# Optimization experiments

Measured on AMD Instinct MI355X. Metric: run time of the kernel, lower is better.

## Reference

```python
import jax, jax.numpy as jnp
import numpy as np

B, E, H, T, O = 128, 512, 1024, 256, 512  # H = 2*E per module


def _uniform(key, shape, k):
    return jax.random.uniform(key, shape, jnp.float32, -k, k)


def setup_inputs() -> dict:
    key = jax.random.key(0)
    ks = jax.random.split(key, 8)
    k_lstm = 1.0 / np.sqrt(H)
    k_fc = 1.0 / np.sqrt(H)
    return {
        "x": jax.random.normal(ks[0], (B, E), jnp.float32),
        "W_ih": _uniform(ks[1], (4 * H, E), k_lstm),   # torch weight_ih_l0, gate order i,f,g,o
        "W_hh": _uniform(ks[2], (4 * H, H), k_lstm),   # torch weight_hh_l0
        "b_ih": _uniform(ks[3], (4 * H,), k_lstm),
        "b_hh": _uniform(ks[4], (4 * H,), k_lstm),
        "fc_w": _uniform(ks[5], (O, H), k_fc),
        "fc_b": _uniform(ks[6], (O,), k_fc),
        "sequence_length": T,
    }


def _lstm_const_input(x, W_ih, W_hh, b_ih, b_hh, T):
    """Single-layer LSTM over `x` repeated T times. Input projection is
    constant across steps, so precompute it once (the headroom insight)."""
    Bb = x.shape[0]
    Hh = W_hh.shape[1]
    z = x @ W_ih.T + (b_ih + b_hh)  # [B, 4H], same every step

    def step(carry, _):
        h, c = carry
        gates = z + h @ W_hh.T                      # [B, 4H]
        i, f, g, o = jnp.split(gates, 4, axis=-1)   # torch gate order i,f,g,o
        i = jax.nn.sigmoid(i)
        f = jax.nn.sigmoid(f)
        g = jnp.tanh(g)
        o = jax.nn.sigmoid(o)
        c = f * c + i * g
        h = o * jnp.tanh(c)
        return (h, c), h

    h0 = jnp.zeros((Bb, Hh), x.dtype)
    (hT, cT), hs = jax.lax.scan(step, (h0, h0), None, length=T)
    return hs, hT  # hs: [T, B, H]


def reference(x, W_ih, W_hh, b_ih, b_hh, fc_w, fc_b, sequence_length):
    hs, hT = _lstm_const_input(x, W_ih, W_hh, b_ih, b_hh, sequence_length)
    seq = jnp.transpose(hs, (1, 0, 2))              # [B, T, H]
    out_sequence = seq @ fc_w.T + fc_b              # [B, T, O]
    # torch: h has shape [num_layers=1, B, H]; h[:, -1, :] picks last batch elem -> [1, H]
    next_state = hT[-1][None, :]
    return out_sequence, next_state
```

## Files before the change

### kernel.cpp

```cpp
#include <hip/hip_runtime.h>
#include <cstdint>
#include <cstddef>

#define BB 128
#define EE 512
#define HH 1024
#define G4 4096
#define OO 512
#define NBLKP 128
#define NTHR 512
#define RED36 36
#define SMEM_BYTES (131072 + BB * RED36 * 4)
#define SPIN_LIMIT (1u << 16)
#define FLAGSTRIDE 16

typedef float f32x4 __attribute__((ext_vector_type(4)));
typedef short s16x8 __attribute__((ext_vector_type(8)));
typedef __bf16 b16x8 __attribute__((ext_vector_type(8)));

template <typename V>
__device__ __forceinline__ auto mfma_try(V a, V b, f32x4 c, int)
    -> decltype(__builtin_amdgcn_mfma_f32_16x16x32_bf16(a, b, c, 0, 0, 0)) {
  return __builtin_amdgcn_mfma_f32_16x16x32_bf16(a, b, c, 0, 0, 0);
}
template <typename V>
__device__ __forceinline__ f32x4 mfma_try(V a, V b, f32x4 c, long) {
  b16x8 ab = __builtin_bit_cast(b16x8, a);
  b16x8 bb = __builtin_bit_cast(b16x8, b);
  return __builtin_amdgcn_mfma_f32_16x16x32_bf16(ab, bb, c, 0, 0, 0);
}
__device__ __forceinline__ f32x4 mfma_bf16(s16x8 a, s16x8 b, f32x4 c) {
  return mfma_try(a, b, c, 0);
}

__device__ __forceinline__ float bf2f(ushort s) {
  unsigned int u = ((unsigned int)s) << 16;
  return __builtin_bit_cast(float, u);
}
__device__ __forceinline__ ushort f2bf(float f) {
  unsigned int u = __builtin_bit_cast(unsigned int, f);
  unsigned int r = (u + 0x7fffu + ((u >> 16) & 1u)) >> 16;
  return (ushort)r;
}
__device__ __forceinline__ float sigm(float x) {
  return 1.0f / (1.0f + __expf(-x));
}
__device__ __forceinline__ void store_short_agent(ushort* p, ushort v) {
  asm volatile("global_store_short %0, %1, off sc1"
               :: "v"(p), "v"((unsigned)v) : "memory");
}

__global__ void __launch_bounds__(256)
convert_split(const float* __restrict__ x, const float* __restrict__ Wih,
              const float* __restrict__ Whh, const float* __restrict__ fcw,
              ushort* __restrict__ xh, ushort* __restrict__ xl,
              ushort* __restrict__ Wihh, ushort* __restrict__ Wihl,
              ushort* __restrict__ Whhh, ushort* __restrict__ Whhl,
              ushort* __restrict__ fcwh, ushort* __restrict__ fcwl,
              unsigned* __restrict__ flags) {
  if (blockIdx.x == 0) {
    for (int j = threadIdx.x; j < NBLKP * FLAGSTRIDE; j += 256) flags[j] = 0u;
  }
  const long n0 = (long)BB * EE;
  const long n1 = n0 + (long)G4 * EE;
  const long n2 = n1 + (long)G4 * HH;
  long i = ((long)blockIdx.x * 256 + threadIdx.x) * 4;
  const float* src;
  ushort *dh, *dl;
  long off;
  if (i < n0) {
    src = x; dh = xh; dl = xl; off = i;
  } else if (i < n1) {
    src = Wih; dh = Wihh; dl = Wihl; off = i - n0;
  } else if (i < n2) {
    src = Whh; dh = Whhh; dl = Whhl; off = i - n1;
  } else {
    src = fcw; dh = fcwh; dl = fcwl; off = i - n2;
  }
  float4 v = *(const float4*)&src[off];
  ushort4 h;
  h.x = f2bf(v.x); h.y = f2bf(v.y); h.z = f2bf(v.z); h.w = f2bf(v.w);
  *(ushort4*)&dh[off] = h;
  ushort4 l;
  l.x = f2bf(v.x - bf2f(h.x));
  l.y = f2bf(v.y - bf2f(h.y));
  l.z = f2bf(v.z - bf2f(h.z));
  l.w = f2bf(v.w - bf2f(h.w));
  *(ushort4*)&dl[off] = l;
}

__global__ void __launch_bounds__(256)
z_split(const ushort* __restrict__ xh, const ushort* __restrict__ xl,
        const ushort* __restrict__ Wihh, const ushort* __restrict__ Wihl,
        const float* __restrict__ bih, const float* __restrict__ bhh,
        float* __restrict__ zbuf) {
  __shared__ alignas(16) ushort Ah[64][72];
  __shared__ alignas(16) ushort Al[64][72];
  __shared__ alignas(16) ushort Bh[32][72];
  __shared__ alignas(16) ushort Bl[32][72];
  const int tid = threadIdx.x, bid = blockIdx.x;
  const int m0 = (bid >> 7) * 64;
  const int hbase = (bid & 127) * 8;
  const int lane = tid & 63, wave = tid >> 6;
  const int wm = wave & 1, wn = wave >> 1;
  const int fr_row = lane & 15, fr_k = (lane >> 4) * 8;
  const f32x4 fz = {0.f, 0.f, 0.f, 0.f};

  f32x4 a0 = fz, a1 = fz;
  for (int kt = 0; kt < EE / 64; ++kt) {
    for (int i = 0; i < 2; ++i) {
      int idx = tid + i * 256;
      int r = idx >> 3, c8 = (idx & 7) * 8;
      int go = (m0 + r) * EE + kt * 64 + c8;
      *(uint4*)&Ah[r][c8] = *(const uint4*)&xh[go];
      *(uint4*)&Al[r][c8] = *(const uint4*)&xl[go];
    }
    {
      int r = tid >> 3, c8 = (tid & 7) * 8;
      int wrow = (r >> 3) * HH + hbase + (r & 7);
      int go = wrow * EE + kt * 64 + c8;
      *(uint4*)&Bh[r][c8] = *(const uint4*)&Wihh[go];
      *(uint4*)&Bl[r][c8] = *(const uint4*)&Wihl[go];
    }
    __syncthreads();
    for (int kc = 0; kc < 2; ++kc) {
      int ko = kc * 32 + fr_k;
      s16x8 bh = *(const s16x8*)&Bh[wn * 16 + fr_row][ko];
      s16x8 bl = *(const s16x8*)&Bl[wn * 16 + fr_row][ko];
      s16x8 f0h = *(const s16x8*)&Ah[wm * 32 + fr_row][ko];
      s16x8 f0l = *(const s16x8*)&Al[wm * 32 + fr_row][ko];
      s16x8 f1h = *(const s16x8*)&Ah[wm * 32 + 16 + fr_row][ko];
      s16x8 f1l = *(const s16x8*)&Al[wm * 32 + 16 + fr_row][ko];
      a0 = mfma_bf16(f0h, bh, a0);
      a0 = mfma_bf16(f0l, bh, a0);
      a0 = mfma_bf16(f0h, bl, a0);
      a1 = mfma_bf16(f1h, bh, a1);
      a1 = mfma_bf16(f1l, bh, a1);
      a1 = mfma_bf16(f1h, bl, a1);
    }
    __syncthreads();
  }
  int jcol = wn * 16 + fr_row;
  int gc = (jcol >> 3) * HH + hbase + (jcol & 7);
  float bias = bih[gc] + bhh[gc];
  int rbase = wm * 32 + (lane >> 4) * 4;
#pragma unroll
  for (int r = 0; r < 4; ++r) {
    zbuf[(size_t)(m0 + rbase + r) * G4 + gc] = a0[r] + bias;
    zbuf[(size_t)(m0 + rbase + 16 + r) * G4 + gc] = a1[r] + bias;
  }
}

__global__ void __launch_bounds__(NTHR, 2)
persist_kernel(const ushort* __restrict__ Whhh, const ushort* __restrict__ Whhl,
               const float* __restrict__ zbuf,
               ushort* __restrict__ hbh, ushort* __restrict__ hbl,
               const ushort* __restrict__ fcwh, const ushort* __restrict__ fcwl,
               const float* __restrict__ fcb, float* __restrict__ out,
               float* __restrict__ out_ns, unsigned* __restrict__ flags,
               int T) {
  (void)hbl;
  extern __shared__ char smem[];
  char* WlB = smem + 65536;
  float* red = (float*)(smem + 131072);

  const int tid = threadIdx.x;
  const int hb = blockIdx.x;
  const int lane = tid & 63;
  const int w = tid >> 6;
  const int fr = lane & 15;
  const int fk8 = (lane >> 4) * 8;
  const int swz = (fr & 7) << 4;
  const f32x4 fz = {0.f, 0.f, 0.f, 0.f};

  for (int i = tid; i < 32 * 128; i += NTHR) {
    int r = i >> 7;
    int cb = (i & 127) * 16;
    int g = r >> 3, c = r & 7;
    size_t go = ((size_t)(g * HH + hb * 8 + c)) * (HH * 2) + (size_t)cb;
    int lofs = r * 2048 + (cb ^ ((r & 7) << 4));
    *(uint4*)(smem + lofs) = *(const uint4*)((const char*)Whhh + go);
    *(uint4*)(WlB + lofs) = *(const uint4*)((const char*)Whhl + go);
  }

  const int crow = tid >> 3, ccol = tid & 7;
  float creg0 = 0.f, creg1 = 0.f;
  size_t zb0 = (size_t)crow * G4 + hb * 8 + ccol;
  size_t zb1 = (size_t)(crow + 64) * G4 + hb * 8 + ccol;
  float zi0 = zbuf[zb0], zf0 = zbuf[zb0 + HH];
  float zg0 = zbuf[zb0 + 2 * HH], zo0 = zbuf[zb0 + 3 * HH];
  float zi1 = zbuf[zb1], zf1 = zbuf[zb1 + HH];
  float zg1 = zbuf[zb1 + 2 * HH], zo1 = zbuf[zb1 + 3 * HH];

  const int m0f = (hb >> 4) * 16;
  const int o0 = (hb & 15) * 32;
  const int wo = w & 1, wkf = w >> 1;
  s16x8 fbh[8], fbl[8];
  {
    size_t base = (size_t)(o0 + wo * 16 + fr) * HH + wkf * 256 + fk8;
#pragma unroll
    for (int j = 0; j < 8; ++j) {
      fbh[j] = *(const s16x8*)&fcwh[base + j * 32];
      fbl[j] = *(const s16x8*)&fcwl[base + j * 32];
    }
  }
  const float fcbv = fcb[o0 + (tid >> 8) * 16 + (tid & 15)];
  __syncthreads();

  for (int t = 0; t <= T; ++t) {
    if (t < T) {
      if (t > 0) {
        const ushort* hph = hbh + (size_t)((t - 1) & 3) * (BB * HH);
        const ushort* ha =
            hph + (size_t)(w * 16 + fr) * 8 + (size_t)(lane >> 4) * (BB * 8);
        f32x4 a0 = fz, a1 = fz;
        s16x8 ph[3][4];
#pragma unroll
        for (int j = 0; j < 4; ++j)
          ph[0][j] = *(const s16x8*)&ha[(j * 4) * (BB * 8)];
#pragma unroll
        for (int j = 0; j < 4; ++j)
          ph[1][j] = *(const s16x8*)&ha[(16 + j * 4) * (BB * 8)];
#pragma unroll
        for (int c = 0; c < 8; ++c) {
          if (c + 2 < 8) {
#pragma unroll
            for (int j = 0; j < 4; ++j) {
              ph[(c + 2) % 3][j] =
                  *(const s16x8*)&ha[((c + 2) * 16 + j * 4) * (BB * 8)];
            }
          }
#pragma unroll
          for (int j = 0; j < 4; ++j) {
            int kk = c * 128 + j * 32 + fk8;
            int sw = (kk * 2) ^ swz;
            int ofs0 = fr * 2048 + sw;
            int ofs1 = (16 + fr) * 2048 + sw;
            s16x8 bh0 = *(const s16x8*)(smem + ofs0);
            s16x8 bl0 = *(const s16x8*)(WlB + ofs0);
            s16x8 bh1 = *(const s16x8*)(smem + ofs1);
            s16x8 bl1 = *(const s16x8*)(WlB + ofs1);
            s16x8 ah = ph[c % 3][j];
            a0 = mfma_bf16(ah, bh0, a0);
            a0 = mfma_bf16(ah, bl0, a0);
            a1 = mfma_bf16(ah, bh1, a1);
            a1 = mfma_bf16(ah, bl1, a1);
          }
        }
        int rrow = w * 16 + (lane >> 4) * 4;
#pragma unroll
        for (int r = 0; r < 4; ++r) {
          red[(rrow + r) * RED36 + fr] = a0[r];
          red[(rrow + r) * RED36 + 16 + fr] = a1[r];
        }
        __syncthreads();
      }
      {
        float gi0 = zi0, gf0 = zf0, gg0 = zg0, go0 = zo0;
        float gi1 = zi1, gf1 = zf1, gg1 = zg1, go1 = zo1;
        if (t > 0) {
          const float* r0 = red + crow * RED36;
          const float* r1 = red + (crow + 64) * RED36;
          gi0 += r0[ccol];      gi1 += r1[ccol];
          gf0 += r0[8 + ccol];  gf1 += r1[8 + ccol];
          gg0 += r0[16 + ccol]; gg1 += r1[16 + ccol];
          go0 += r0[24 + ccol]; go1 += r1[24 + ccol];
        }
        float iv0 = sigm(gi0), fv0 = sigm(gf0), gv0 = tanhf(gg0), ov0 = sigm(go0);
        float iv1 = sigm(gi1), fv1 = sigm(gf1), gv1 = tanhf(gg1), ov1 = sigm(go1);
        creg0 = fv0 * creg0 + iv0 * gv0;
        creg1 = fv1 * creg1 + iv1 * gv1;
        float hv0 = ov0 * tanhf(creg0);
        float hv1 = ov1 * tanhf(creg1);
        ushort hh0 = f2bf(hv0);
        ushort hh1 = f2bf(hv1);
        size_t hob = (size_t)(t & 3) * (BB * HH) + (size_t)hb * (BB * 8);
        store_short_agent(hbh + hob + tid, hh0);
        store_short_agent(hbh + hob + 512 + tid, hh1);
        if (t == T - 1 && crow == 63) out_ns[hb * 8 + ccol] = hv1;
      }
      __syncthreads();
      if (tid == 0) {
        __hip_atomic_store(&flags[hb * FLAGSTRIDE], (unsigned)(t + 1),
                           __ATOMIC_RELAXED, __HIP_MEMORY_SCOPE_AGENT);
      }
    }
    if (t > 0) {
      const ushort* hch = hbh + (size_t)((t - 1) & 3) * (BB * HH);
      const ushort* hca =
          hch + (size_t)(m0f + fr) * 8 + (size_t)(lane >> 4) * (BB * 8);
      f32x4 acc = fz;
#pragma unroll
      for (int j = 0; j < 8; ++j) {
        s16x8 afh = *(const s16x8*)&hca[(wkf * 32 + j * 4) * (BB * 8)];
        acc = mfma_bf16(afh, fbh[j], acc);
        acc = mfma_bf16(afh, fbl[j], acc);
      }
      int rb = (lane >> 4) * 4;
      float* rp = red + (wkf * 2 + wo) * 256;
#pragma unroll
      for (int r = 0; r < 4; ++r) rp[(rb + r) * 16 + fr] = acc[r];
      __syncthreads();
      {
        int wo2 = tid >> 8, row = (tid >> 4) & 15, col = tid & 15;
        float s = fcbv;
#pragma unroll
        for (int k = 0; k < 4; ++k)
          s += red[(k * 2 + wo2) * 256 + row * 16 + col];
        out[((size_t)(m0f + row) * T + (t - 1)) * OO + o0 + wo2 * 16 + col] = s;
      }
    }
    if (t < T) {
      if (tid < 64) __builtin_amdgcn_fence(__ATOMIC_ACQUIRE, "agent");
      __syncthreads();
      if (tid < NBLKP) {
        const int i = tid;
        unsigned tgt = (unsigned)(t + 1);
        unsigned spins = 0;
        while (__hip_atomic_load(&flags[i * FLAGSTRIDE], __ATOMIC_RELAXED,
                                 __HIP_MEMORY_SCOPE_AGENT) < tgt) {
          __builtin_amdgcn_s_sleep(1);
          if (++spins > SPIN_LIMIT) break;
        }
        if ((i >> 3) == (hb >> 3)) {
          const uint* ph2 =
              (const uint*)(hbh + (size_t)(t & 3) * (BB * HH) + i * (BB * 8));
          unsigned acc2 = 0;
#pragma unroll
          for (int k2 = 0; k2 < 32; ++k2) acc2 += ph2[k2 * 16];
          asm volatile("" :: "v"(acc2));
        }
      }
      __syncthreads();
    }
  }
}

extern "C" void kernel_launch(void* const* d_in, const int* in_sizes, int n_in,
                              void* d_out, int out_size, void* d_ws,
                              size_t ws_size, hipStream_t stream) {
  (void)ws_size;
  const float *x = nullptr, *Wih = nullptr, *Whh = nullptr, *fcw = nullptr;
  const float *bih = nullptr, *bhh = nullptr, *fcb = nullptr;
  for (int i = 0; i < n_in; ++i) {
    int s = in_sizes[i];
    const float* p = (const float*)d_in[i];
    if (s == BB * EE && !x) x = p;
    else if (s == G4 * EE && !Wih) Wih = p;
    else if (s == G4 * HH && !Whh) Whh = p;
    else if (s == OO * HH && !fcw) fcw = p;
    else if (s == G4 && !bih) bih = p;
    else if (s == G4 && !bhh) bhh = p;
    else if (s == OO && !fcb) fcb = p;
  }
  if (!x || !Wih || !Whh || !fcw || !bih || !bhh || !fcb) return;

  int T = 0;
  if (out_size >= BB * OO && (out_size - HH) % (BB * OO) == 0 &&
      (out_size - HH) / (BB * OO) >= 1) {
    T = (out_size - HH) / (BB * OO);
  } else if (out_size % (BB * OO) == 0) {
    T = out_size / (BB * OO);
  }
  if (T < 1 || T > 16384) return;

  float* out = (float*)d_out;
  float* out_ns = out + (size_t)BB * T * OO;

  ushort* xh = (ushort*)d_ws;
  ushort* xl = xh + (size_t)BB * EE;
  ushort* Wihh = xl + (size_t)BB * EE;
  ushort* Wihl = Wihh + (size_t)G4 * EE;
  ushort* Whhh = Wihl + (size_t)G4 * EE;
  ushort* Whhl = Whhh + (size_t)G4 * HH;
  ushort* fcwh = Whhl + (size_t)G4 * HH;
  ushort* fcwl = fcwh + (size_t)OO * HH;
  ushort* hbh = fcwl + (size_t)OO * HH;
  ushort* hbl = hbh + (size_t)4 * BB * HH;
  float* zbuf = (float*)(hbl + (size_t)4 * BB * HH);
  unsigned* flags = (unsigned*)(zbuf + (size_t)BB * G4);

  {
    long total = (long)BB * EE + (long)G4 * EE + (long)G4 * HH + (long)OO * HH;
    int cblocks = (int)(total / 4 / 256);
    hipLaunchKernelGGL(convert_split, dim3(cblocks), dim3(256), 0, stream, x,
                       Wih, Whh, fcw, xh, xl, Wihh, Wihl, Whhh, Whhl, fcwh,
                       fcwl, flags);
  }
  hipLaunchKernelGGL(z_split, dim3(256), dim3(256), 0, stream, xh, xl, Wihh,
                     Wihl, bih, bhh, zbuf);

  static int attr_set = 0;
  if (!attr_set) {
    (void)hipFuncSetAttribute((const void*)persist_kernel,
                              hipFuncAttributeMaxDynamicSharedMemorySize,
                              SMEM_BYTES);
    attr_set = 1;
  }
  hipLaunchKernelGGL(persist_kernel, dim3(NBLKP), dim3(NTHR), SMEM_BYTES,
                     stream, Whhh, Whhl, zbuf, hbh, hbl, fcwh, fcwl, fcb, out,
                     out_ns, flags, T);
}
```

Before: 1.911 ms.

## Specialize warps: half do recurrent GEMM, half do FC projection concurrently

```diff
diff --git a/kernel.cpp b/kernel.cpp
--- a/kernel.cpp
+++ b/kernel.cpp
@@ -10,7 +10,7 @@
 #define NBLKP 128
 #define NTHR 512
 #define RED36 36
-#define SMEM_BYTES (131072 + BB * RED36 * 4)
+#define SMEM_BYTES (131072 + BB * RED36 * 4 + 4096)
 #define SPIN_LIMIT (1u << 16)
 #define FLAGSTRIDE 16
 
@@ -163,13 +163,15 @@
   extern __shared__ char smem[];
   char* WlB = smem + 65536;
   float* red = (float*)(smem + 131072);
+  float* fred = (float*)(smem + 131072 + BB * RED36 * 4);
 
   const int tid = threadIdx.x;
   const int hb = blockIdx.x;
   const int lane = tid & 63;
   const int w = tid >> 6;
   const int fr = lane & 15;
-  const int fk8 = (lane >> 4) * 8;
+  const int q = lane >> 4;
+  const int fk8 = q * 8;
   const int swz = (fr & 7) << 4;
   const f32x4 fz = {0.f, 0.f, 0.f, 0.f};
 
@@ -194,123 +196,123 @@
 
   const int m0f = (hb >> 4) * 16;
   const int o0 = (hb & 15) * 32;
-  const int wo = w & 1, wkf = w >> 1;
-  s16x8 fbh[8], fbl[8];
-  {
-    size_t base = (size_t)(o0 + wo * 16 + fr) * HH + wkf * 256 + fk8;
-#pragma unroll
-    for (int j = 0; j < 8; ++j) {
-      fbh[j] = *(const s16x8*)&fcwh[base + j * 32];
-      fbl[j] = *(const s16x8*)&fcwl[base + j * 32];
-    }
-  }
+  const int fw = w - 4;
+  const int fwo = fw & 1, fkh = fw >> 1;
   const float fcbv = fcb[o0 + (tid >> 8) * 16 + (tid & 15)];
   __syncthreads();
 
   for (int t = 0; t <= T; ++t) {
-    if (t < T) {
-      if (t > 0) {
-        const ushort* hph = hbh + (size_t)((t - 1) & 3) * (BB * HH);
-        const ushort* ha =
-            hph + (size_t)(w * 16 + fr) * 8 + (size_t)(lane >> 4) * (BB * 8);
-        f32x4 a0 = fz, a1 = fz;
-        s16x8 ph[3][4];
-#pragma unroll
-        for (int j = 0; j < 4; ++j)
-          ph[0][j] = *(const s16x8*)&ha[(j * 4) * (BB * 8)];
-#pragma unroll
-        for (int j = 0; j < 4; ++j)
-          ph[1][j] = *(const s16x8*)&ha[(16 + j * 4) * (BB * 8)];
-#pragma unroll
-        for (int c = 0; c < 8; ++c) {
-          if (c + 2 < 8) {
+    if (t > 0) {
+      if (w < 4) {
+        if (t < T) {
+          const ushort* hph = hbh + (size_t)((t - 1) & 3) * (BB * HH);
+          const ushort* ha0 =
+              hph + (size_t)(w * 32 + fr) * 8 + (size_t)q * (BB * 8);
+          const ushort* ha1 = ha0 + 128;
+          f32x4 a00 = fz, a01 = fz, a10 = fz, a11 = fz;
+          s16x8 p0[2][4], p1[2][4];
+#pragma unroll
+          for (int j = 0; j < 4; ++j) {
+            p0[0][j] = *(const s16x8*)&ha0[(j * 4) * (BB * 8)];
+            p1[0][j] = *(const s16x8*)&ha1[(j * 4) * (BB * 8)];
+          }
+#pragma unroll
+          for (int c = 0; c < 8; ++c) {
+            if (c < 7) {
+#pragma unroll
+              for (int j = 0; j < 4; ++j) {
+                p0[(c + 1) & 1][j] =
+                    *(const s16x8*)&ha0[((c + 1) * 16 + j * 4) * (BB * 8)];
+                p1[(c + 1) & 1][j] =
+                    *(const s16x8*)&ha1[((c + 1) * 16 + j * 4) * (BB * 8)];
+              }
+            }
 #pragma unroll
             for (int j = 0; j < 4; ++j) {
-              ph[(c + 2) % 3][j] =
-                  *(const s16x8*)&ha[((c + 2) * 16 + j * 4) * (BB * 8)];
+              int kk = c * 128 + j * 32 + fk8;
+              int sw = (kk * 2) ^ swz;
+              int ofs0 = fr * 2048 + sw;
+              int ofs1 = (16 + fr) * 2048 + sw;
+              s16x8 bh0 = *(const s16x8*)(smem + ofs0);
+              s16x8 bl0 = *(const s16x8*)(WlB + ofs0);
+              s16x8 bh1 = *(const s16x8*)(smem + ofs1);
+              s16x8 bl1 = *(const s16x8*)(WlB + ofs1);
+              s16x8 ah0 = p0[c & 1][j], ah1 = p1[c & 1][j];
+              a00 = mfma_bf16(ah0, bh0, a00);
+              a00 = mfma_bf16(ah0, bl0, a00);
+              a01 = mfma_bf16(ah0, bh1, a01);
+              a01 = mfma_bf16(ah0, bl1, a01);
+              a10 = mfma_bf16(ah1, bh0, a10);
+              a10 = mfma_bf16(ah1, bl0, a10);
+              a11 = mfma_bf16(ah1, bh1, a11);
+              a11 = mfma_bf16(ah1, bl1, a11);
             }
           }
-#pragma unroll
-          for (int j = 0; j < 4; ++j) {
-            int kk = c * 128 + j * 32 + fk8;
-            int sw = (kk * 2) ^ swz;
-            int ofs0 = fr * 2048 + sw;
-            int ofs1 = (16 + fr) * 2048 + sw;
-            s16x8 bh0 = *(const s16x8*)(smem + ofs0);
-            s16x8 bl0 = *(const s16x8*)(WlB + ofs0);
-            s16x8 bh1 = *(const s16x8*)(smem + ofs1);
-            s16x8 bl1 = *(const s16x8*)(WlB + ofs1);
-            s16x8 ah = ph[c % 3][j];
-            a0 = mfma_bf16(ah, bh0, a0);
-            a0 = mfma_bf16(ah, bl0, a0);
-            a1 = mfma_bf16(ah, bh1, a1);
-            a1 = mfma_bf16(ah, bl1, a1);
+          int rr = w * 32 + q * 4;
+#pragma unroll
+          for (int r = 0; r < 4; ++r) {
+            red[(rr + r) * RED36 + fr] = a00[r];
+            red[(rr + r) * RED36 + 16 + fr] = a01[r];
+            red[(rr + 16 + r) * RED36 + fr] = a10[r];
+            red[(rr + 16 + r) * RED36 + 16 + fr] = a11[r];
           }
         }
-        int rrow = w * 16 + (lane >> 4) * 4;
-#pragma unroll
-        for (int r = 0; r < 4; ++r) {
-          red[(rrow + r) * RED36 + fr] = a0[r];
-          red[(rrow + r) * RED36 + 16 + fr] = a1[r];
+      } else {
+        const ushort* hch = hbh + (size_t)((t - 1) & 3) * (BB * HH);
+        const ushort* hca = hch + (size_t)(m0f + fr) * 8 +
+                            (size_t)(fkh * 64 + q) * (BB * 8);
+        size_t wb = (size_t)(o0 + fwo * 16 + fr) * HH + (size_t)fkh * 512 + fk8;
+        f32x4 acc = fz;
+#pragma unroll
+        for (int j = 0; j < 16; ++j) {
+          s16x8 afh = *(const s16x8*)&hca[(j * 4) * (BB * 8)];
+          s16x8 wfh = *(const s16x8*)&fcwh[wb + j * 32];
+          s16x8 wfl = *(const s16x8*)&fcwl[wb + j * 32];
+          acc = mfma_bf16(afh, wfh, acc);
+          acc = mfma_bf16(afh, wfl, acc);
         }
-        __syncthreads();
+#pragma unroll
+        for (int r = 0; r < 4; ++r)
+          fred[fw * 256 + (q * 4 + r) * 16 + fr] = acc[r];
       }
-      {
-        float gi0 = zi0, gf0 = zf0, gg0 = zg0, go0 = zo0;
-        float gi1 = zi1, gf1 = zf1, gg1 = zg1, go1 = zo1;
-        if (t > 0) {
-          const float* r0 = red + crow * RED36;
-          const float* r1 = red + (crow + 64) * RED36;
-          gi0 += r0[ccol];      gi1 += r1[ccol];
-          gf0 += r0[8 + ccol];  gf1 += r1[8 + ccol];
-          gg0 += r0[16 + ccol]; gg1 += r1[16 + ccol];
-          go0 += r0[24 + ccol]; go1 += r1[24 + ccol];
-        }
-        float iv0 = sigm(gi0), fv0 = sigm(gf0), gv0 = tanhf(gg0), ov0 = sigm(go0);
-        float iv1 = sigm(gi1), fv1 = sigm(gf1), gv1 = tanhf(gg1), ov1 = sigm(go1);
-        creg0 = fv0 * creg0 + iv0 * gv0;
-        creg1 = fv1 * creg1 + iv1 * gv1;
-        float hv0 = ov0 * tanhf(creg0);
-        float hv1 = ov1 * tanhf(creg1);
-        ushort hh0 = f2bf(hv0);
-        ushort hh1 = f2bf(hv1);
-        size_t hob = (size_t)(t & 3) * (BB * HH) + (size_t)hb * (BB * 8);
-        store_short_agent(hbh + hob + tid, hh0);
-        store_short_agent(hbh + hob + 512 + tid, hh1);
-        if (t == T - 1 && crow == 63) out_ns[hb * 8 + ccol] = hv1;
+    }
+    __syncthreads();
+    if (t < T) {
+      float gi0 = zi0, gf0 = zf0, gg0 = zg0, go0 = zo0;
+      float gi1 = zi1, gf1 = zf1, gg1 = zg1, go1 = zo1;
+      if (t > 0) {
+        const float* r0 = red + crow * RED36;
+        const float* r1 = red + (crow + 64) * RED36;
+        gi0 += r0[ccol];      gi1 += r1[ccol];
+        gf0 += r0[8 + ccol];  gf1 += r1[8 + ccol];
+        gg0 += r0[16 + ccol]; gg1 += r1[16 + ccol];
+        go0 += r0[24 + ccol]; go1 += r1[24 + ccol];
       }
+      float iv0 = sigm(gi0), fv0 = sigm(gf0), gv0 = tanhf(gg0), ov0 = sigm(go0);
+      float iv1 = sigm(gi1), fv1 = sigm(gf1), gv1 = tanhf(gg1), ov1 = sigm(go1);
+      creg0 = fv0 * creg0 + iv0 * gv0;
+      creg1 = fv1 * creg1 + iv1 * gv1;
+      float hv0 = ov0 * tanhf(creg0);
+      float hv1 = ov1 * tanhf(creg1);
+      ushort hh0 = f2bf(hv0);
+      ushort hh1 = f2bf(hv1);
+      size_t hob = (size_t)(t & 3) * (BB * HH) + (size_t)hb * (BB * 8);
+      store_short_agent(hbh + hob + tid, hh0);
+      store_short_agent(hbh + hob + 512 + tid, hh1);
+      if (t == T - 1 && crow == 63) out_ns[hb * 8 + ccol] = hv1;
+    }
+    if (t > 0) {
+      int wo2 = tid >> 8, row = (tid >> 4) & 15, col = tid & 15;
+      float s = fcbv + fred[wo2 * 256 + row * 16 + col] +
+                fred[(2 + wo2) * 256 + row * 16 + col];
+      out[((size_t)(m0f + row) * T + (t - 1)) * OO + o0 + wo2 * 16 + col] = s;
+    }
+    if (t < T) {
       __syncthreads();
       if (tid == 0) {
         __hip_atomic_store(&flags[hb * FLAGSTRIDE], (unsigned)(t + 1),
                            __ATOMIC_RELAXED, __HIP_MEMORY_SCOPE_AGENT);
       }
-    }
-    if (t > 0) {
-      const ushort* hch = hbh + (size_t)((t - 1) & 3) * (BB * HH);
-      const ushort* hca =
-          hch + (size_t)(m0f + fr) * 8 + (size_t)(lane >> 4) * (BB * 8);
-      f32x4 acc = fz;
-#pragma unroll
-      for (int j = 0; j < 8; ++j) {
-        s16x8 afh = *(const s16x8*)&hca[(wkf * 32 + j * 4) * (BB * 8)];
-        acc = mfma_bf16(afh, fbh[j], acc);
-        acc = mfma_bf16(afh, fbl[j], acc);
-      }
-      int rb = (lane >> 4) * 4;
-      float* rp = red + (wkf * 2 + wo) * 256;
-#pragma unroll
-      for (int r = 0; r < 4; ++r) rp[(rb + r) * 16 + fr] = acc[r];
-      __syncthreads();
-      {
-        int wo2 = tid >> 8, row = (tid >> 4) & 15, col = tid & 15;
-        float s = fcbv;
-#pragma unroll
-        for (int k = 0; k < 4; ++k)
-          s += red[(k * 2 + wo2) * 256 + row * 16 + col];
-        out[((size_t)(m0f + row) * T + (t - 1)) * OO + o0 + wo2 * 16 + col] = s;
-      }
-    }
-    if (t < T) {
       if (tid < 64) __builtin_amdgcn_fence(__ATOMIC_ACQUIRE, "agent");
       __syncthreads();
       if (tid < NBLKP) {
```

Result: slower. 3.270 ms (+71.1%).
